# Performance work log

Hardware: AMD Instinct MI355X
Metric: run time of the kernel (lower is better)

## Reference

```python
import jax, jax.numpy as jnp
import numpy as np

B, S, H, NH = 2, 1024, 1024, 16
SE, E = 512, 1024
NEXP, TOPK, FF = 8, 2, 2048
HD = H // NH
EPS = 1e-6
THETA = 10000.0
NEG = -1e9


def _rms(x, w):
    return x * jax.lax.rsqrt(jnp.mean(x * x, axis=-1, keepdims=True) + EPS) * w


def _rope(q, k, pos):
    # q,k: [B,S,NH,HD]; pos: [B,S] int
    inv = 1.0 / (THETA ** (jnp.arange(0, HD, 2, dtype=jnp.float32) / HD))
    f = pos[..., None].astype(jnp.float32) * inv            # [B,S,HD/2]
    emb = jnp.concatenate([f, f], axis=-1)                  # [B,S,HD]
    cos = jnp.cos(emb)[:, :, None, :]
    sin = jnp.sin(emb)[:, :, None, :]
    def rot(x):
        x1, x2 = jnp.split(x, 2, axis=-1)
        return jnp.concatenate([-x2, x1], axis=-1)
    return q * cos + rot(q) * sin, k * cos + rot(k) * sin


def _forward(hidden_states, encoder_hidden_states,
             in_ln_w, wq, wk, wv, wo,
             c_norm_w, cq_w, cq_b, ck_w, ck_b, cv_w, cv_b, co_w, co_b,
             post_ln_w, gate_w, w1, w2, w3,
             position_ids, encoder_attention_mask):
    x = hidden_states

    # ---- self-attention (RMSNorm pre-norm, RoPE, causal) ----
    res = x
    h = _rms(x, in_ln_w)
    q = (h @ wq.T).reshape(B, S, NH, HD)
    k = (h @ wk.T).reshape(B, S, NH, HD)
    v = (h @ wv.T).reshape(B, S, NH, HD)
    q, k = _rope(q, k, position_ids)
    scores = jnp.einsum('bqhd,bkhd->bhqk', q, k) / np.sqrt(HD)
    causal = jnp.tril(jnp.ones((S, S), dtype=bool))
    scores = jnp.where(causal, scores, NEG)
    attn = jax.nn.softmax(scores, axis=-1)
    o = jnp.einsum('bhqk,bkhd->bqhd', attn, v).reshape(B, S, H) @ wo.T
    x = res + o

    # ---- cross-attention block (RMSNorm, MHA with kdim=vdim=E, bias) ----
    res = x
    h = _rms(x, c_norm_w)
    cq = (h @ cq_w.T + cq_b).reshape(B, S, NH, HD)
    ck = (encoder_hidden_states @ ck_w.T + ck_b).reshape(B, SE, NH, HD)
    cv = (encoder_hidden_states @ cv_w.T + cv_b).reshape(B, SE, NH, HD)
    sc = jnp.einsum('bqhd,bkhd->bhqk', cq, ck) / np.sqrt(HD)
    pad = (encoder_attention_mask == 0)                     # key_padding_mask
    sc = jnp.where(pad[:, None, None, :], NEG, sc)
    ca = jax.nn.softmax(sc, axis=-1)
    o = jnp.einsum('bhqk,bkhd->bqhd', ca, cv).reshape(B, S, H) @ co_w.T + co_b
    x = res + o

    # ---- block-sparse MoE FFN (top-2 routing, SwiGLU experts) ----
    res = x
    h = _rms(x, post_ln_w).reshape(-1, H)                   # [T,H], T=B*S
    logits = h @ gate_w.T                                    # [T,NEXP]
    probs = jax.nn.softmax(logits, axis=-1)
    topv, topi = jax.lax.top_k(probs, TOPK)                  # [T,TOPK]
    topv = topv / jnp.sum(topv, axis=-1, keepdims=True)
    out = jnp.zeros_like(h)
    for e in range(NEXP):  # fixed small expert loop
        we = jnp.sum(jnp.where(topi == e, topv, 0.0), axis=-1)   # [T]
        ff = (jax.nn.silu(h @ w1[e].T) * (h @ w3[e].T)) @ w2[e].T
        out = out + we[:, None] * ff
    x = res + out.reshape(B, S, H)
    return x


def setup_inputs() -> dict:
    key = jax.random.key(0)
    ks = jax.random.split(key, 24)
    sc = 0.02
    d = {
        'hidden_states': jax.random.normal(ks[0], (B, S, H), jnp.float32),
        'position_ids': jnp.broadcast_to(jnp.arange(S, dtype=jnp.int64), (B, S)),
        'encoder_hidden_states': jax.random.normal(ks[1], (B, SE, E), jnp.float32),
        'encoder_attention_mask': jnp.ones((B, SE), jnp.int64),
        'in_ln_w': jnp.ones((H,), jnp.float32),
        'wq': jax.random.normal(ks[2], (H, H), jnp.float32) * sc,
        'wk': jax.random.normal(ks[3], (H, H), jnp.float32) * sc,
        'wv': jax.random.normal(ks[4], (H, H), jnp.float32) * sc,
        'wo': jax.random.normal(ks[5], (H, H), jnp.float32) * sc,
        'c_norm_w': jnp.ones((H,), jnp.float32),
        'cq_w': jax.random.normal(ks[6], (H, H), jnp.float32) * sc,
        'cq_b': jnp.zeros((H,), jnp.float32),
        'ck_w': jax.random.normal(ks[7], (H, E), jnp.float32) * sc,
        'ck_b': jnp.zeros((H,), jnp.float32),
        'cv_w': jax.random.normal(ks[8], (H, E), jnp.float32) * sc,
        'cv_b': jnp.zeros((H,), jnp.float32),
        'co_w': jax.random.normal(ks[9], (H, H), jnp.float32) * sc,
        'co_b': jnp.zeros((H,), jnp.float32),
        'post_ln_w': jnp.ones((H,), jnp.float32),
        'gate_w': jax.random.normal(ks[10], (NEXP, H), jnp.float32) * sc,
        'w1': jax.random.normal(ks[11], (NEXP, FF, H), jnp.float32) * sc,
        'w2': jax.random.normal(ks[12], (NEXP, H, FF), jnp.float32) * sc,
        'w3': jax.random.normal(ks[13], (NEXP, FF, H), jnp.float32) * sc,
    }
    return d


def reference(hidden_states, position_ids, encoder_hidden_states, encoder_attention_mask,
              in_ln_w, wq, wk, wv, wo,
              c_norm_w, cq_w, cq_b, ck_w, ck_b, cv_w, cv_b, co_w, co_b,
              post_ln_w, gate_w, w1, w2, w3):
    return _forward(hidden_states, encoder_hidden_states,
                    in_ln_w, wq, wk, wv, wo,
                    c_norm_w, cq_w, cq_b, ck_w, ck_b, cv_w, cv_b, co_w, co_b,
                    post_ln_w, gate_w, w1, w2, w3,
                    position_ids, encoder_attention_mask)
```

## Files before the change

### kernel.cpp

```cpp
#include <hip/hip_runtime.h>

#define B_    2
#define S_    1024
#define H_    1024
#define NH_   16
#define HD_   64
#define SE_   512
#define E_    1024
#define NEXP_ 8
#define FF_   2048
#define T_    (B_*S_)
#define TE_   (B_*SE_)
#define PERM_MAX 6400
#define MAXRT 48

typedef short v8s __attribute__((ext_vector_type(8)));
typedef short v4s __attribute__((ext_vector_type(4)));
typedef float v4f __attribute__((ext_vector_type(4)));
typedef _Float16 v8h __attribute__((ext_vector_type(8)));
typedef _Float16 v4h __attribute__((ext_vector_type(4)));

__device__ __forceinline__ unsigned short f2b(float f) {
  unsigned int u = __float_as_uint(f);
  u = (u + 0x7FFFu + ((u >> 16) & 1u)) >> 16;
  return (unsigned short)u;
}
__device__ __forceinline__ float b2f(unsigned short h) {
  return __uint_as_float(((unsigned int)h) << 16);
}

__device__ __forceinline__ void g2l16(const void* g, void* l) {
  __builtin_amdgcn_global_load_lds(
      (const __attribute__((address_space(1))) unsigned int*)g,
      (__attribute__((address_space(3))) unsigned int*)l, 16, 0, 0);
}

__global__ void detect_kern(const int* __restrict__ pos, const int* __restrict__ msk,
                            int* __restrict__ flags) {
  if (threadIdx.x == 0) {
    flags[0] = (pos[1] == 1) ? 0 : 1;
    flags[1] = (msk[1] == 1) ? 0 : 1;
  }
}

__global__ __launch_bounds__(256)
void split_kern(const float* __restrict__ x, _Float16* __restrict__ oh,
                _Float16* __restrict__ ol, int n8) {
  int i = blockIdx.x * 256 + threadIdx.x;
  if (i >= n8) return;
  v4f a = *(const v4f*)&x[i * 8];
  v4f b = *(const v4f*)&x[i * 8 + 4];
  v8h hv, lv;
  #pragma unroll
  for (int j = 0; j < 8; ++j) {
    float v = j < 4 ? a[j] : b[j - 4];
    _Float16 hh = (_Float16)v;
    hv[j] = hh; lv[j] = (_Float16)(v - (float)hh);
  }
  *(v8h*)&oh[i * 8] = hv;
  *(v8h*)&ol[i * 8] = lv;
}

__global__ __launch_bounds__(256)
void rmsnorm_hl_kern(const float* __restrict__ x, const float* __restrict__ w,
                     _Float16* __restrict__ yh, _Float16* __restrict__ yl) {
  int row = blockIdx.x, tid = threadIdx.x;
  const float* xr = x + (long)row * 1024;
  v4f v = *(const v4f*)&xr[tid * 4];
  float ss = v[0]*v[0] + v[1]*v[1] + v[2]*v[2] + v[3]*v[3];
  #pragma unroll
  for (int off = 32; off; off >>= 1) ss += __shfl_xor(ss, off);
  __shared__ float sw[4];
  if ((tid & 63) == 0) sw[tid >> 6] = ss;
  __syncthreads();
  float tot = sw[0] + sw[1] + sw[2] + sw[3];
  float rs = rsqrtf(tot * (1.0f / 1024.0f) + 1e-6f);
  const float* wr = w + tid * 4;
  v4h oh, ol;
  #pragma unroll
  for (int j = 0; j < 4; ++j) {
    float f = v[j] * rs * wr[j];
    _Float16 hh = (_Float16)f;
    oh[j] = hh; ol[j] = (_Float16)(f - (float)hh);
  }
  *(v4h*)&yh[(long)row * 1024 + tid * 4] = oh;
  *(v4h*)&yl[(long)row * 1024 + tid * 4] = ol;
}

__global__ __launch_bounds__(256)
void rmsnorm_kern(const float* __restrict__ x, const float* __restrict__ w,
                  unsigned short* __restrict__ y) {
  int row = blockIdx.x, tid = threadIdx.x;
  const float* xr = x + (long)row * 1024;
  v4f v = *(const v4f*)&xr[tid * 4];
  float ss = v[0]*v[0] + v[1]*v[1] + v[2]*v[2] + v[3]*v[3];
  #pragma unroll
  for (int off = 32; off; off >>= 1) ss += __shfl_xor(ss, off);
  __shared__ float sw[4];
  if ((tid & 63) == 0) sw[tid >> 6] = ss;
  __syncthreads();
  float tot = sw[0] + sw[1] + sw[2] + sw[3];
  float rs = rsqrtf(tot * (1.0f / 1024.0f) + 1e-6f);
  const float* wr = w + tid * 4;
  v4s o;
  #pragma unroll
  for (int j = 0; j < 4; ++j) o[j] = (short)f2b(v[j] * rs * wr[j]);
  *(v4s*)&y[(long)row * 1024 + tid * 4] = o;
}

__global__ __launch_bounds__(256)
void cvt_kern(const float* __restrict__ x, unsigned short* __restrict__ y, int n4) {
  int i = blockIdx.x * 256 + threadIdx.x;
  if (i >= n4) return;
  v4f v = *(const v4f*)&x[i * 4];
  v4s o;
  #pragma unroll
  for (int j = 0; j < 4; ++j) o[j] = (short)f2b(v[j]);
  *(v4s*)&y[i * 4] = o;
}

__global__ __launch_bounds__(256)
void rope_split_kern(float* __restrict__ q, const float* __restrict__ k,
                     _Float16* __restrict__ kh, _Float16* __restrict__ kl,
                     const int* __restrict__ pos, const int* __restrict__ flags) {
  int g = blockIdx.x * 256 + threadIdx.x;
  int d = g & 31;
  int h = (g >> 5) & 15;
  int s = (g >> 9) & (S_ - 1);
  int b = g >> 19;
  long base = (((long)(b * S_ + s)) * NH_ + h) * HD_;
  int pidx = b * S_ + s;
  int pv = pos[flags[0] ? (pidx << 1) : pidx];
  float p = (float)pv;
  float inv = powf(10000.0f, -(float)d * (1.0f / 32.0f));
  float f = p * inv;
  float sn = sinf(f), cs = cosf(f);
  float q1 = q[base + d], q2 = q[base + d + 32];
  q[base + d]      = q1 * cs - q2 * sn;
  q[base + d + 32] = q2 * cs + q1 * sn;
  float k1 = k[base + d], k2 = k[base + d + 32];
  float kr1 = k1 * cs - k2 * sn;
  float kr2 = k2 * cs + k1 * sn;
  _Float16 hh = (_Float16)kr1;
  kh[base + d] = hh; kl[base + d] = (_Float16)(kr1 - (float)hh);
  hh = (_Float16)kr2;
  kh[base + d + 32] = hh; kl[base + d + 32] = (_Float16)(kr2 - (float)hh);
}

__global__ __launch_bounds__(256)
void vtrans_kern(const float* __restrict__ vf, _Float16* __restrict__ vth,
                 _Float16* __restrict__ vtl, int Sk) {
  int kb = blockIdx.x, bh = blockIdx.y;
  int b = bh >> 4, h = bh & 15;
  int t = threadIdx.x;
  __shared__ float tile[64][65];
  int key = t >> 2, dsub = (t & 3) * 16;
  const float* src = vf + (((long)(b * Sk + kb * 64 + key)) * NH_ + h) * HD_ + dsub;
  #pragma unroll
  for (int j = 0; j < 16; j += 4) *(v4f*)&tile[key][dsub + j] = *(const v4f*)&src[j];
  __syncthreads();
  int d = t >> 2, ksub = (t & 3) * 16;
  v8h hv0, lv0, hv1, lv1;
  #pragma unroll
  for (int j = 0; j < 16; ++j) {
    float v = tile[ksub + j][d];
    _Float16 hh = (_Float16)v;
    if (j < 8) { hv0[j] = hh; lv0[j] = (_Float16)(v - (float)hh); }
    else       { hv1[j - 8] = hh; lv1[j - 8] = (_Float16)(v - (float)hh); }
  }
  long ob = (((long)(b * NH_ + h)) * HD_ + d) * Sk + kb * 64 + ksub;
  *(v8h*)&vth[ob] = hv0; *(v8h*)&vth[ob + 8] = hv1;
  *(v8h*)&vtl[ob] = lv0; *(v8h*)&vtl[ob + 8] = lv1;
}

struct ZArg {
  const _Float16 *Ah, *Al, *Bh, *Bl;
  const float *bias, *resid;
  float *Cf;
  _Float16 *Ch, *Cl;
  int M;
};

__global__ __launch_bounds__(256)
void gemm_hl(ZArg z0, ZArg z1, ZArg z2, int K) {
  ZArg za = blockIdx.z == 0 ? z0 : (blockIdx.z == 1 ? z1 : z2);
  int row0 = blockIdx.x * 128;
  if (row0 >= za.M) return;
  int col0 = blockIdx.y * 64;
  int tid = threadIdx.x, lane = tid & 63, w = tid >> 6;
  int lr = lane & 15, lg = lane >> 4;
  int wr = w >> 1, wc = w & 1;

  __shared__ _Float16 Ah_s[128 * 32], Al_s[128 * 32];
  __shared__ _Float16 Bh_s[64 * 32], Bl_s[64 * 32];

  int av0 = w * 64 + lane, av1 = (w + 4) * 64 + lane;
  int ar0 = av0 >> 2, as0 = av0 & 3;
  int ar1 = av1 >> 2, as1 = av1 & 3;
  int bv = w * 64 + lane;
  int br = bv >> 2, bs = bv & 3;
  const _Float16* ga0h = za.Ah + (long)(row0 + ar0) * K + as0 * 8;
  const _Float16* ga0l = za.Al + (long)(row0 + ar0) * K + as0 * 8;
  const _Float16* ga1h = za.Ah + (long)(row0 + ar1) * K + as1 * 8;
  const _Float16* ga1l = za.Al + (long)(row0 + ar1) * K + as1 * 8;
  const _Float16* gbh  = za.Bh + (long)(col0 + br) * K + bs * 8;
  const _Float16* gbl  = za.Bl + (long)(col0 + br) * K + bs * 8;

  v4f acc[4][2] = {};

  for (int k0 = 0; k0 < K; k0 += 32) {
    __syncthreads();
    g2l16(ga0h + k0, (char*)Ah_s + w * 1024);
    g2l16(ga1h + k0, (char*)Ah_s + (w + 4) * 1024);
    g2l16(ga0l + k0, (char*)Al_s + w * 1024);
    g2l16(ga1l + k0, (char*)Al_s + (w + 4) * 1024);
    g2l16(gbh + k0, (char*)Bh_s + w * 1024);
    g2l16(gbl + k0, (char*)Bl_s + w * 1024);
    __syncthreads();

    v8h ah[4], al[4], bh[2], bl[2];
    #pragma unroll
    for (int m = 0; m < 4; ++m) {
      int off = (wr * 64 + m * 16 + lr) * 64 + lg * 16;
      ah[m] = *(const v8h*)((char*)Ah_s + off);
      al[m] = *(const v8h*)((char*)Al_s + off);
    }
    #pragma unroll
    for (int n = 0; n < 2; ++n) {
      int off = (wc * 32 + n * 16 + lr) * 64 + lg * 16;
      bh[n] = *(const v8h*)((char*)Bh_s + off);
      bl[n] = *(const v8h*)((char*)Bl_s + off);
    }
    #pragma unroll
    for (int m = 0; m < 4; ++m)
      #pragma unroll
      for (int n = 0; n < 2; ++n) {
        acc[m][n] = __builtin_amdgcn_mfma_f32_16x16x32_f16(ah[m], bh[n], acc[m][n], 0, 0, 0);
        acc[m][n] = __builtin_amdgcn_mfma_f32_16x16x32_f16(ah[m], bl[n], acc[m][n], 0, 0, 0);
        acc[m][n] = __builtin_amdgcn_mfma_f32_16x16x32_f16(al[m], bh[n], acc[m][n], 0, 0, 0);
      }
  }

  #pragma unroll
  for (int m = 0; m < 4; ++m) {
    int rbase = row0 + wr * 64 + m * 16 + lg * 4;
    #pragma unroll
    for (int n = 0; n < 2; ++n) {
      int gcol = col0 + wc * 32 + n * 16 + lr;
      float bb = za.bias ? za.bias[gcol] : 0.0f;
      #pragma unroll
      for (int rr = 0; rr < 4; ++rr) {
        long idx = (long)(rbase + rr) * 1024 + gcol;
        float v = acc[m][n][rr] + bb;
        if (za.Cf) {
          za.Cf[idx] = za.resid ? (za.resid[idx] + v) : v;
        } else {
          _Float16 hh = (_Float16)v;
          za.Ch[idx] = hh;
          za.Cl[idx] = (_Float16)(v - (float)hh);
        }
      }
    }
  }
}

template<bool CAUSAL>
__global__ __launch_bounds__(256)
void attn_hl(const float* __restrict__ Q,
             const _Float16* __restrict__ Khg, const _Float16* __restrict__ Klg,
             const _Float16* __restrict__ Vhg, const _Float16* __restrict__ Vlg,
             _Float16* __restrict__ Oh, _Float16* __restrict__ Ol,
             const int* __restrict__ mask, const int* __restrict__ flags,
             int Sq, int Sk, float qscale) {
  int qt = blockIdx.x, bh = blockIdx.y;
  int b = bh >> 4, h = bh & 15;
  int tid = threadIdx.x, lane = tid & 63, w = tid >> 6;
  int lr = lane & 15, lg = lane >> 4;
  int q0 = qt * 64;
  int mf = (!CAUSAL && mask) ? flags[1] : 0;
  int swz = lr & 7;

  __shared__ _Float16 Kh_s[64 * 64], Kl_s[64 * 64];
  __shared__ _Float16 Vh_s[64 * 64], Vl_s[64 * 64];
  __shared__ _Float16 Psh[4][16][72], Psl[4][16][72];

  v8h qh[2], ql[2];
  {
    long qbase = ((long)(b * Sq + q0 + w * 16 + lr) * NH_ + h) * HD_;
    #pragma unroll
    for (int kk = 0; kk < 2; ++kk) {
      v4f f0 = *(const v4f*)&Q[qbase + kk * 32 + lg * 8];
      v4f f1 = *(const v4f*)&Q[qbase + kk * 32 + lg * 8 + 4];
      #pragma unroll
      for (int j = 0; j < 8; ++j) {
        float f = (j < 4 ? f0[j] : f1[j - 4]) * qscale;
        _Float16 hh = (_Float16)f;
        qh[kk][j] = hh;
        ql[kk][j] = (_Float16)(f - (float)hh);
      }
    }
  }
  v4f of[4] = {};
  float m4[4], l4[4];
  #pragma unroll
  for (int i = 0; i < 4; ++i) { m4[i] = -3e38f; l4[i] = 0.0f; }

  int nkt = CAUSAL ? (qt + 1) : (Sk >> 6);
  for (int kt = 0; kt < nkt; ++kt) {
    __syncthreads();
    #pragma unroll
    for (int i = 0; i < 2; ++i) {
      int c = w + i * 4;
      int v = c * 64 + lane;
      int row = v >> 3, c8 = v & 7;
      int sc = (c8 ^ (row & 7)) << 3;
      long kb = ((long)(b * Sk + kt * 64 + row) * NH_ + h) * HD_ + sc;
      g2l16(Khg + kb, (char*)Kh_s + c * 1024);
      g2l16(Klg + kb, (char*)Kl_s + c * 1024);
      long vb = ((long)(b * NH_ + h) * HD_ + row) * Sk + kt * 64 + sc;
      g2l16(Vhg + vb, (char*)Vh_s + c * 1024);
      g2l16(Vlg + vb, (char*)Vl_s + c * 1024);
    }
    __syncthreads();

    v4f sf[4] = {};
    #pragma unroll
    for (int kk = 0; kk < 2; ++kk)
      #pragma unroll
      for (int n = 0; n < 4; ++n) {
        int off = (n * 16 + lr) * 128 + ((((kk << 2) | lg) ^ swz) << 4);
        v8h kbh = *(const v8h*)((char*)Kh_s + off);
        v8h kbl = *(const v8h*)((char*)Kl_s + off);
        sf[n] = __builtin_amdgcn_mfma_f32_16x16x32_f16(qh[kk], kbh, sf[n], 0, 0, 0);
        sf[n] = __builtin_amdgcn_mfma_f32_16x16x32_f16(qh[kk], kbl, sf[n], 0, 0, 0);
        sf[n] = __builtin_amdgcn_mfma_f32_16x16x32_f16(ql[kk], kbh, sf[n], 0, 0, 0);
      }

    if constexpr (CAUSAL) {
      if (kt == qt) {
        #pragma unroll
        for (int n = 0; n < 4; ++n) {
          int kcol = kt * 64 + n * 16 + lr;
          #pragma unroll
          for (int rr = 0; rr < 4; ++rr) {
            int qr = q0 + w * 16 + lg * 4 + rr;
            if (kcol > qr) sf[n][rr] = -1e9f;
          }
        }
      }
    } else {
      if (mask) {
        #pragma unroll
        for (int n = 0; n < 4; ++n) {
          int kcol = kt * 64 + n * 16 + lr;
          int mi = b * Sk + kcol;
          if (mask[mf ? (mi << 1) : mi] == 0) {
            #pragma unroll
            for (int rr = 0; rr < 4; ++rr) sf[n][rr] = -1e9f;
          }
        }
      }
    }

    float al[4];
    #pragma unroll
    for (int rr = 0; rr < 4; ++rr) {
      float mx = fmaxf(fmaxf(sf[0][rr], sf[1][rr]), fmaxf(sf[2][rr], sf[3][rr]));
      #pragma unroll
      for (int off = 8; off; off >>= 1) mx = fmaxf(mx, __shfl_xor(mx, off));
      float mn = fmaxf(m4[rr], mx);
      al[rr] = __expf(m4[rr] - mn);
      m4[rr] = mn;
      float rs = 0.0f;
      #pragma unroll
      for (int n = 0; n < 4; ++n) {
        float pv = __expf(sf[n][rr] - mn);
        sf[n][rr] = pv;
        rs += pv;
      }
      #pragma unroll
      for (int off = 8; off; off >>= 1) rs += __shfl_xor(rs, off);
      l4[rr] = l4[rr] * al[rr] + rs;
    }

    #pragma unroll
    for (int n = 0; n < 4; ++n)
      #pragma unroll
      for (int rr = 0; rr < 4; ++rr) {
        of[n][rr] *= al[rr];
        float pv = sf[n][rr];
        _Float16 ph = (_Float16)pv;
        Psh[w][lg * 4 + rr][n * 16 + lr] = ph;
        Psl[w][lg * 4 + rr][n * 16 + lr] = (_Float16)(pv - (float)ph);
      }
    __syncthreads();

    #pragma unroll
    for (int kc = 0; kc < 2; ++kc) {
      v8h pah = *(const v8h*)&Psh[w][lr][kc * 32 + lg * 8];
      v8h pal = *(const v8h*)&Psl[w][lr][kc * 32 + lg * 8];
      #pragma unroll
      for (int n = 0; n < 4; ++n) {
        int off = (n * 16 + lr) * 128 + ((((kc << 2) | lg) ^ swz) << 4);
        v8h vbh = *(const v8h*)((char*)Vh_s + off);
        v8h vbl = *(const v8h*)((char*)Vl_s + off);
        of[n] = __builtin_amdgcn_mfma_f32_16x16x32_f16(pah, vbh, of[n], 0, 0, 0);
        of[n] = __builtin_amdgcn_mfma_f32_16x16x32_f16(pah, vbl, of[n], 0, 0, 0);
        of[n] = __builtin_amdgcn_mfma_f32_16x16x32_f16(pal, vbh, of[n], 0, 0, 0);
      }
    }
  }

  #pragma unroll
  for (int rr = 0; rr < 4; ++rr) {
    int qr = q0 + w * 16 + lg * 4 + rr;
    float inv = 1.0f / l4[rr];
    long ob = (long)(b * Sq + qr) * 1024 + h * 64;
    #pragma unroll
    for (int n = 0; n < 4; ++n) {
      float v = of[n][rr] * inv;
      _Float16 hh = (_Float16)v;
      Oh[ob + n * 16 + lr] = hh;
      Ol[ob + n * 16 + lr] = (_Float16)(v - (float)hh);
    }
  }
}

__global__ __launch_bounds__(256)
void moe_gemm1(const unsigned short* __restrict__ A,
               const unsigned short* __restrict__ B1,
               const unsigned short* __restrict__ B2,
               unsigned short* __restrict__ Cb,
               const int* __restrict__ tm_e, const int* __restrict__ tm_slot,
               const int* __restrict__ ntl, const int* __restrict__ perm) {
  int tile = blockIdx.x;
  if (tile >= ntl[0]) return;
  int e = tm_e[tile];
  int row0 = tm_slot[tile];
  const unsigned short* Bp1 = B1 + (long)e * (FF_ * H_);
  const unsigned short* Bp2 = B2 + (long)e * (FF_ * H_);
  int col0 = blockIdx.y * 64;
  int tid = threadIdx.x, lane = tid & 63, w = tid >> 6;
  int lr = lane & 15, lg = lane >> 4;
  int wr = w >> 1, wc = w & 1;

  __shared__ unsigned short As[128 * 32];
  __shared__ unsigned short Bs1[64 * 32];
  __shared__ unsigned short Bs2[64 * 32];

  const unsigned short* ga[2];
  #pragma unroll
  for (int i = 0; i < 2; ++i) {
    int c = i * 256 + tid;
    int r = c >> 2, sub = c & 3;
    int tok = perm[row0 + r];
    ga[i] = A + (long)(tok < 0 ? 0 : tok) * H_ + sub * 8;
  }
  int rb = tid >> 2, subb = (tid & 3) * 8;
  const unsigned short* gb1 = Bp1 + (long)(col0 + rb) * H_ + subb;
  const unsigned short* gb2 = Bp2 + (long)(col0 + rb) * H_ + subb;

  v4f acc[4][2] = {};
  v4f acc2[4][2] = {};

  for (int k0 = 0; k0 < H_; k0 += 32) {
    __syncthreads();
    #pragma unroll
    for (int i = 0; i < 2; ++i)
      g2l16(ga[i] + k0, As + (size_t)(i * 256 + w * 64) * 8);
    g2l16(gb1 + k0, Bs1 + (size_t)(w * 64) * 8);
    g2l16(gb2 + k0, Bs2 + (size_t)(w * 64) * 8);
    __syncthreads();

    v8s a[4], b[2];
    #pragma unroll
    for (int m = 0; m < 4; ++m) a[m] = *(const v8s*)&As[(wr * 64 + m * 16 + lr) * 32 + lg * 8];
    #pragma unroll
    for (int n = 0; n < 2; ++n) b[n] = *(const v8s*)&Bs1[(wc * 32 + n * 16 + lr) * 32 + lg * 8];
    #pragma unroll
    for (int m = 0; m < 4; ++m)
      #pragma unroll
      for (int n = 0; n < 2; ++n)
        acc[m][n] = __builtin_amdgcn_mfma_f32_16x16x32_bf16(a[m], b[n], acc[m][n], 0, 0, 0);
    #pragma unroll
    for (int n = 0; n < 2; ++n) b[n] = *(const v8s*)&Bs2[(wc * 32 + n * 16 + lr) * 32 + lg * 8];
    #pragma unroll
    for (int m = 0; m < 4; ++m)
      #pragma unroll
      for (int n = 0; n < 2; ++n)
        acc2[m][n] = __builtin_amdgcn_mfma_f32_16x16x32_bf16(a[m], b[n], acc2[m][n], 0, 0, 0);
  }

  #pragma unroll
  for (int m = 0; m < 4; ++m) {
    int grow = row0 + wr * 64 + m * 16 + lg * 4;
    #pragma unroll
    for (int n = 0; n < 2; ++n) {
      int gcol = col0 + wc * 32 + n * 16 + lr;
      #pragma unroll
      for (int rr = 0; rr < 4; ++rr) {
        float v = acc[m][n][rr];
        float g = v / (1.0f + __expf(-v));
        Cb[(long)(grow + rr) * FF_ + gcol] = f2b(g * acc2[m][n][rr]);
      }
    }
  }
}

__global__ __launch_bounds__(256)
void moe_gemm2(const unsigned short* __restrict__ A,
               const unsigned short* __restrict__ B,
               float* __restrict__ Cf,
               const int* __restrict__ tm_e, const int* __restrict__ tm_slot,
               const int* __restrict__ ntl,
               const int* __restrict__ perm, const float* __restrict__ pwgt) {
  int tile = blockIdx.x;
  if (tile >= ntl[0]) return;
  int e = tm_e[tile];
  int row0 = tm_slot[tile];
  const unsigned short* Bp = B + (long)e * (H_ * FF_);
  int col0 = blockIdx.y * 128;
  int tid = threadIdx.x, lane = tid & 63, w = tid >> 6;
  int lr = lane & 15, lg = lane >> 4;
  int wr = w >> 1, wc = w & 1;

  __shared__ unsigned short As[128 * 32];
  __shared__ unsigned short Bs[128 * 32];

  const unsigned short* ga[2];
  const unsigned short* gb[2];
  #pragma unroll
  for (int i = 0; i < 2; ++i) {
    int c = i * 256 + tid;
    int r = c >> 2, sub = c & 3;
    ga[i] = A + (long)(row0 + r) * FF_ + sub * 8;
    gb[i] = Bp + (long)(col0 + r) * FF_ + sub * 8;
  }

  v4f acc[4][4] = {};

  for (int k0 = 0; k0 < FF_; k0 += 32) {
    __syncthreads();
    #pragma unroll
    for (int i = 0; i < 2; ++i) {
      g2l16(ga[i] + k0, As + (size_t)(i * 256 + w * 64) * 8);
      g2l16(gb[i] + k0, Bs + (size_t)(i * 256 + w * 64) * 8);
    }
    __syncthreads();

    v8s a[4], b[4];
    #pragma unroll
    for (int m = 0; m < 4; ++m) a[m] = *(const v8s*)&As[(wr * 64 + m * 16 + lr) * 32 + lg * 8];
    #pragma unroll
    for (int n = 0; n < 4; ++n) b[n] = *(const v8s*)&Bs[(wc * 64 + n * 16 + lr) * 32 + lg * 8];
    #pragma unroll
    for (int m = 0; m < 4; ++m)
      #pragma unroll
      for (int n = 0; n < 4; ++n)
        acc[m][n] = __builtin_amdgcn_mfma_f32_16x16x32_bf16(a[m], b[n], acc[m][n], 0, 0, 0);
  }

  #pragma unroll
  for (int m = 0; m < 4; ++m) {
    int grow = row0 + wr * 64 + m * 16 + lg * 4;
    #pragma unroll
    for (int rr = 0; rr < 4; ++rr) {
      int tok = perm[grow + rr];
      if (tok < 0) continue;
      float pw = pwgt[grow + rr];
      #pragma unroll
      for (int n = 0; n < 4; ++n) {
        int gcol = col0 + wc * 64 + n * 16 + lr;
        atomicAdd(&Cf[(long)tok * H_ + gcol], acc[m][n][rr] * pw);
      }
    }
  }
}

__global__ __launch_bounds__(64)
void router_kern(const float* __restrict__ x, const float* __restrict__ w,
                 const float* __restrict__ gw,
                 int* __restrict__ topi, float* __restrict__ topw,
                 int* __restrict__ counts) {
  int t = blockIdx.x, lane = threadIdx.x;
  const float* xr = x + (long)t * 1024;
  float vals[16];
  float ss = 0.0f;
  #pragma unroll
  for (int i = 0; i < 16; ++i) { float v = xr[lane + i * 64]; vals[i] = v; ss += v * v; }
  #pragma unroll
  for (int off = 32; off; off >>= 1) ss += __shfl_xor(ss, off);
  float rs = rsqrtf(ss * (1.0f / 1024.0f) + 1e-6f);
  #pragma unroll
  for (int i = 0; i < 16; ++i) vals[i] *= rs * w[lane + i * 64];
  float lgts[8];
  #pragma unroll
  for (int e = 0; e < 8; ++e) {
    const float* g = gw + e * 1024;
    float s = 0.0f;
    #pragma unroll
    for (int i = 0; i < 16; ++i) s += vals[i] * g[lane + i * 64];
    #pragma unroll
    for (int off = 32; off; off >>= 1) s += __shfl_xor(s, off);
    lgts[e] = s;
  }
  int i1 = 0; float l1 = lgts[0];
  #pragma unroll
  for (int e = 1; e < 8; ++e) if (lgts[e] > l1) { l1 = lgts[e]; i1 = e; }
  int i2 = -1; float l2 = -3e38f;
  #pragma unroll
  for (int e = 0; e < 8; ++e) if (e != i1 && lgts[e] > l2) { l2 = lgts[e]; i2 = e; }
  float w1 = 1.0f / (1.0f + __expf(l2 - l1));
  if (lane == 0) {
    topi[t * 2] = i1; topi[t * 2 + 1] = i2;
    topw[t * 2] = w1; topw[t * 2 + 1] = 1.0f - w1;
    atomicAdd(&counts[i1], 1);
    atomicAdd(&counts[i2], 1);
  }
}

__global__ __launch_bounds__(256)
void finalize_kern(const int* __restrict__ counts, int* __restrict__ poff,
                   int* __restrict__ tm_e, int* __restrict__ tm_slot,
                   int* __restrict__ ntl, int* __restrict__ perm) {
  __shared__ int stot;
  if (threadIdx.x == 0) {
    int off = 0, nt = 0;
    for (int e = 0; e < 8; ++e) {
      poff[e] = off;
      int c = counts[e];
      int ntE = (c + 127) >> 7;
      for (int i = 0; i < ntE; ++i) { tm_e[nt] = e; tm_slot[nt] = off + i * 128; ++nt; }
      off += ntE * 128;
    }
    ntl[0] = nt; ntl[1] = off;
    stot = off;
  }
  __syncthreads();
  for (int s = threadIdx.x; s < stot; s += 256) perm[s] = -1;
}

__global__ __launch_bounds__(256)
void scatter_kern(const int* __restrict__ topi, const float* __restrict__ topw,
                  const int* __restrict__ poff, int* __restrict__ cursor,
                  int* __restrict__ perm, float* __restrict__ pwgt) {
  int t = blockIdx.x * 256 + threadIdx.x;
  if (t >= T_) return;
  #pragma unroll
  for (int kk = 0; kk < 2; ++kk) {
    int e = topi[t * 2 + kk];
    int pos = atomicAdd(&cursor[e], 1);
    int slot = poff[e] + pos;
    perm[slot] = t;
    pwgt[slot] = topw[t * 2 + kk];
  }
}

extern "C" void kernel_launch(void* const* d_in, const int* in_sizes, int n_in,
                              void* d_out, int out_size, void* d_ws, size_t ws_size,
                              hipStream_t stream) {
  (void)in_sizes; (void)n_in; (void)out_size; (void)ws_size;
  const float* x_in  = (const float*)d_in[0];
  const int*  posids = (const int*)d_in[1];
  const float* enc   = (const float*)d_in[2];
  const int*  emask  = (const int*)d_in[3];
  const float* inln  = (const float*)d_in[4];
  const float* wq    = (const float*)d_in[5];
  const float* wk    = (const float*)d_in[6];
  const float* wv    = (const float*)d_in[7];
  const float* wo    = (const float*)d_in[8];
  const float* cnorm = (const float*)d_in[9];
  const float* cqw   = (const float*)d_in[10];
  const float* cqb   = (const float*)d_in[11];
  const float* ckw   = (const float*)d_in[12];
  const float* ckb   = (const float*)d_in[13];
  const float* cvw   = (const float*)d_in[14];
  const float* cvb   = (const float*)d_in[15];
  const float* cow   = (const float*)d_in[16];
  const float* cob   = (const float*)d_in[17];
  const float* pln   = (const float*)d_in[18];
  const float* gatew = (const float*)d_in[19];
  const float* w1    = (const float*)d_in[20];
  const float* w2    = (const float*)d_in[21];
  const float* w3    = (const float*)d_in[22];
  float* out = (float*)d_out;

  char* p = (char*)d_ws;
  auto alloc = [&](size_t bytes) -> char* {
    char* r = p;
    p += (bytes + 255) & ~(size_t)255;
    return r;
  };
  const size_t MB = 1024 * 1024;
  char* A1 = alloc(4 * MB);
  char* A2 = alloc(4 * MB);
  char* Bq = alloc(8 * MB);
  char* Bk = alloc(8 * MB);
  char* Bv = alloc(8 * MB);
  char* C1 = alloc(4 * MB);
  char* C2 = alloc(4 * MB);
  char* D1 = alloc(4 * MB);
  char* D2 = alloc(4 * MB);
  float* x1 = (float*)alloc(8 * MB);
  float* x2 = (float*)alloc(8 * MB);
  unsigned short* h3b = (unsigned short*)alloc(4 * MB);
  _Float16* ench = (_Float16*)alloc(2 * MB);
  _Float16* encl = (_Float16*)alloc(2 * MB);
  int*   meta    = (int*)alloc(4 * (8 + 8 + 8 + 2 + 2 + MAXRT + MAXRT));
  int*   counts  = meta;
  int*   cursor  = meta + 8;
  int*   poff    = meta + 16;
  int*   ntl     = meta + 24;
  int*   flags   = meta + 26;
  int*   tm_e    = meta + 28;
  int*   tm_slot = meta + 28 + MAXRT;
  int*   topi    = (int*)alloc((size_t)T_ * 2 * 4);
  float* topw    = (float*)alloc((size_t)T_ * 2 * 4);
  int*   perm    = (int*)alloc((size_t)PERM_MAX * 4);
  float* pwgt    = (float*)alloc((size_t)PERM_MAX * 4);
  unsigned short* w1b = (unsigned short*)alloc((size_t)NEXP_ * FF_ * H_ * 2);
  unsigned short* w3b = (unsigned short*)alloc((size_t)NEXP_ * FF_ * H_ * 2);
  unsigned short* w2b = (unsigned short*)alloc((size_t)NEXP_ * H_ * FF_ * 2);

  _Float16 *hh = (_Float16*)A1, *hl = (_Float16*)A2;
  _Float16 *oh = (_Float16*)A1, *ol = (_Float16*)A2;
  _Float16 *ckh = (_Float16*)A1, *ckl = (_Float16*)A2;
  float* qf = (float*)Bq;  float* cqf = (float*)Bq;
  float* kf = (float*)Bk;
  _Float16 *cvth = (_Float16*)Bk, *cvtl = (_Float16*)(Bk + 4 * MB);
  float* vf = (float*)Bv;  float* cvf = (float*)Bv;
  _Float16 *kh = (_Float16*)C1, *kl = (_Float16*)C2;
  _Float16 *h2h = (_Float16*)C1, *h2l = (_Float16*)C2;
  _Float16 *vth = (_Float16*)D1, *vtl = (_Float16*)D2;
  _Float16 *coh = (_Float16*)D1, *col = (_Float16*)D2;
  unsigned short* ffh = (unsigned short*)Bq;
  _Float16* wsp = (_Float16*)w1b;
  auto wsph = [&](int i) { return wsp + (size_t)i * 2097152; };
  auto wspl = [&](int i) { return wsp + (size_t)i * 2097152 + 1048576; };

  dim3 blk(256);
  const int WN8 = H_ * H_ / 8;

  detect_kern<<<1, 64, 0, stream>>>(posids, emask, flags);

  const float* wlist[8] = {wq, wk, wv, wo, cqw, ckw, cvw, cow};
  for (int i = 0; i < 8; ++i)
    split_kern<<<(WN8 + 255) / 256, blk, 0, stream>>>(wlist[i], wsph(i), wspl(i), WN8);
  split_kern<<<(TE_ * E_ / 8 + 255) / 256, blk, 0, stream>>>(enc, ench, encl, TE_ * E_ / 8);

  rmsnorm_hl_kern<<<T_, blk, 0, stream>>>(x_in, inln, hh, hl);
  {
    ZArg zq = {hh, hl, wsph(0), wspl(0), nullptr, nullptr, qf, nullptr, nullptr, 2048};
    ZArg zk = {hh, hl, wsph(1), wspl(1), nullptr, nullptr, kf, nullptr, nullptr, 2048};
    ZArg zv = {hh, hl, wsph(2), wspl(2), nullptr, nullptr, vf, nullptr, nullptr, 2048};
    gemm_hl<<<dim3(16, 16, 3), blk, 0, stream>>>(zq, zk, zv, 1024);
  }
  rope_split_kern<<<(B_ * S_ * NH_ * 32) / 256, blk, 0, stream>>>(qf, kf, kh, kl, posids, flags);
  vtrans_kern<<<dim3(16, 32), blk, 0, stream>>>(vf, vth, vtl, 1024);
  attn_hl<true><<<dim3(16, 32), blk, 0, stream>>>(
      qf, kh, kl, vth, vtl, oh, ol, nullptr, flags, 1024, 1024, 0.125f);
  {
    ZArg zo = {oh, ol, wsph(3), wspl(3), nullptr, x_in, x1, nullptr, nullptr, 2048};
    gemm_hl<<<dim3(16, 16, 1), blk, 0, stream>>>(zo, zo, zo, 1024);
  }

  rmsnorm_hl_kern<<<T_, blk, 0, stream>>>(x1, cnorm, h2h, h2l);
  {
    ZArg zcq = {h2h, h2l, wsph(4), wspl(4), cqb, nullptr, cqf, nullptr, nullptr, 2048};
    ZArg zck = {ench, encl, wsph(5), wspl(5), ckb, nullptr, nullptr, ckh, ckl, 1024};
    ZArg zcv = {ench, encl, wsph(6), wspl(6), cvb, nullptr, cvf, nullptr, nullptr, 1024};
    gemm_hl<<<dim3(16, 16, 3), blk, 0, stream>>>(zcq, zck, zcv, 1024);
  }
  vtrans_kern<<<dim3(8, 32), blk, 0, stream>>>(cvf, cvth, cvtl, 512);
  attn_hl<false><<<dim3(16, 32), blk, 0, stream>>>(
      cqf, ckh, ckl, cvth, cvtl, coh, col, emask, flags, 1024, 512, 0.125f);
  {
    ZArg zco = {coh, col, wsph(7), wspl(7), cob, x1, x2, nullptr, nullptr, 2048};
    gemm_hl<<<dim3(16, 16, 1), blk, 0, stream>>>(zco, zco, zco, 1024);
  }

  cvt_kern<<<(NEXP_ * FF_ * H_ / 4 + 255) / 256, blk, 0, stream>>>(w1, w1b, NEXP_ * FF_ * H_ / 4);
  cvt_kern<<<(NEXP_ * FF_ * H_ / 4 + 255) / 256, blk, 0, stream>>>(w3, w3b, NEXP_ * FF_ * H_ / 4);
  cvt_kern<<<(NEXP_ * H_ * FF_ / 4 + 255) / 256, blk, 0, stream>>>(w2, w2b, NEXP_ * H_ * FF_ / 4);
  rmsnorm_kern<<<T_, blk, 0, stream>>>(x2, pln, h3b);
  hipMemsetAsync(meta, 0, 64, stream);
  router_kern<<<T_, dim3(64), 0, stream>>>(x2, pln, gatew, topi, topw, counts);
  finalize_kern<<<1, blk, 0, stream>>>(counts, poff, tm_e, tm_slot, ntl, perm);
  scatter_kern<<<(T_ + 255) / 256, blk, 0, stream>>>(topi, topw, poff, cursor, perm, pwgt);
  moe_gemm1<<<dim3(MAXRT, FF_ / 64), blk, 0, stream>>>(
      h3b, w1b, w3b, ffh, tm_e, tm_slot, ntl, perm);
  hipMemcpyAsync(out, x2, (size_t)T_ * H_ * 4, hipMemcpyDeviceToDevice, stream);
  moe_gemm2<<<dim3(MAXRT, H_ / 128), blk, 0, stream>>>(
      ffh, w2b, out, tm_e, tm_slot, ntl, perm, pwgt);
}
```

Measured before the change: 590.8 us.

## Swizzle LDS layouts and double MoE tile rows to 256 with 512-thread blocks

Applies an XOR swizzle to the 16-byte chunk index in the shared-memory layouts of gemm_hl and both MoE GEMMs, so the MFMA operand reads hit fewer LDS bank conflicts. The MoE GEMMs move to 512-thread blocks covering 256-row expert tiles, with finalize and the grid bound changed to match. Each weight tile is then reused across twice as many tokens, cutting repeated weight traffic. The cost is more padding per expert tile (up to 255 rows) and half as many blocks in the MoE launches, which can leave fewer blocks to fill the GPU.

```diff
diff --git a/kernel.cpp b/kernel.cpp
--- a/kernel.cpp
+++ b/kernel.cpp
@@ -12,7 +12,7 @@
 #define T_    (B_*S_)
 #define TE_   (B_*SE_)
 #define PERM_MAX 6400
-#define MAXRT 48
+#define MAXRT 24
 
 typedef short v8s __attribute__((ext_vector_type(8)));
 typedef short v4s __attribute__((ext_vector_type(4)));
@@ -190,15 +190,16 @@
   int tid = threadIdx.x, lane = tid & 63, w = tid >> 6;
   int lr = lane & 15, lg = lane >> 4;
   int wr = w >> 1, wc = w & 1;
+  int rsw = (lr >> 1) & 3;
 
   __shared__ _Float16 Ah_s[128 * 32], Al_s[128 * 32];
   __shared__ _Float16 Bh_s[64 * 32], Bl_s[64 * 32];
 
   int av0 = w * 64 + lane, av1 = (w + 4) * 64 + lane;
-  int ar0 = av0 >> 2, as0 = av0 & 3;
-  int ar1 = av1 >> 2, as1 = av1 & 3;
+  int ar0 = av0 >> 2, as0 = (av0 & 3) ^ ((ar0 >> 1) & 3);
+  int ar1 = av1 >> 2, as1 = (av1 & 3) ^ ((ar1 >> 1) & 3);
   int bv = w * 64 + lane;
-  int br = bv >> 2, bs = bv & 3;
+  int br = bv >> 2, bs = (bv & 3) ^ ((br >> 1) & 3);
   const _Float16* ga0h = za.Ah + (long)(row0 + ar0) * K + as0 * 8;
   const _Float16* ga0l = za.Al + (long)(row0 + ar0) * K + as0 * 8;
   const _Float16* ga1h = za.Ah + (long)(row0 + ar1) * K + as1 * 8;
@@ -221,13 +222,13 @@
     v8h ah[4], al[4], bh[2], bl[2];
     #pragma unroll
     for (int m = 0; m < 4; ++m) {
-      int off = (wr * 64 + m * 16 + lr) * 64 + lg * 16;
+      int off = (wr * 64 + m * 16 + lr) * 64 + ((lg ^ rsw) << 4);
       ah[m] = *(const v8h*)((char*)Ah_s + off);
       al[m] = *(const v8h*)((char*)Al_s + off);
     }
     #pragma unroll
     for (int n = 0; n < 2; ++n) {
-      int off = (wc * 32 + n * 16 + lr) * 64 + lg * 16;
+      int off = (wc * 32 + n * 16 + lr) * 64 + ((lg ^ rsw) << 4);
       bh[n] = *(const v8h*)((char*)Bh_s + off);
       bl[n] = *(const v8h*)((char*)Bl_s + off);
     }
@@ -426,7 +427,7 @@
   }
 }
 
-__global__ __launch_bounds__(256)
+__global__ __launch_bounds__(512)
 void moe_gemm1(const unsigned short* __restrict__ A,
                const unsigned short* __restrict__ B1,
                const unsigned short* __restrict__ B2,
@@ -443,22 +444,24 @@
   int tid = threadIdx.x, lane = tid & 63, w = tid >> 6;
   int lr = lane & 15, lg = lane >> 4;
   int wr = w >> 1, wc = w & 1;
-
-  __shared__ unsigned short As[128 * 32];
+  int rsw = (lr >> 1) & 3;
+
+  __shared__ unsigned short As[256 * 32];
   __shared__ unsigned short Bs1[64 * 32];
   __shared__ unsigned short Bs2[64 * 32];
 
   const unsigned short* ga[2];
   #pragma unroll
   for (int i = 0; i < 2; ++i) {
-    int c = i * 256 + tid;
-    int r = c >> 2, sub = c & 3;
+    int c = i * 512 + tid;
+    int r = c >> 2, sub = (c & 3) ^ ((r >> 1) & 3);
     int tok = perm[row0 + r];
     ga[i] = A + (long)(tok < 0 ? 0 : tok) * H_ + sub * 8;
   }
-  int rb = tid >> 2, subb = (tid & 3) * 8;
-  const unsigned short* gb1 = Bp1 + (long)(col0 + rb) * H_ + subb;
-  const unsigned short* gb2 = Bp2 + (long)(col0 + rb) * H_ + subb;
+  int bc = tid & 255;
+  int rb = bc >> 2, sb = (bc & 3) ^ ((rb >> 1) & 3);
+  const unsigned short* gB = (tid < 256 ? Bp1 : Bp2) + (long)(col0 + rb) * H_ + sb * 8;
+  unsigned short* lB = (tid < 256 ? Bs1 : Bs2) + (size_t)((w & 3) * 64) * 8;
 
   v4f acc[4][2] = {};
   v4f acc2[4][2] = {};
@@ -467,28 +470,26 @@
     __syncthreads();
     #pragma unroll
     for (int i = 0; i < 2; ++i)
-      g2l16(ga[i] + k0, As + (size_t)(i * 256 + w * 64) * 8);
-    g2l16(gb1 + k0, Bs1 + (size_t)(w * 64) * 8);
-    g2l16(gb2 + k0, Bs2 + (size_t)(w * 64) * 8);
-    __syncthreads();
-
-    v8s a[4], b[2];
-    #pragma unroll
-    for (int m = 0; m < 4; ++m) a[m] = *(const v8s*)&As[(wr * 64 + m * 16 + lr) * 32 + lg * 8];
-    #pragma unroll
-    for (int n = 0; n < 2; ++n) b[n] = *(const v8s*)&Bs1[(wc * 32 + n * 16 + lr) * 32 + lg * 8];
+      g2l16(ga[i] + k0, As + (size_t)(i * 512 + w * 64) * 8);
+    g2l16(gB + k0, lB);
+    __syncthreads();
+
+    v8s a[4], b1[2], b2[2];
     #pragma unroll
     for (int m = 0; m < 4; ++m)
-      #pragma unroll
-      for (int n = 0; n < 2; ++n)
-        acc[m][n] = __builtin_amdgcn_mfma_f32_16x16x32_bf16(a[m], b[n], acc[m][n], 0, 0, 0);
-    #pragma unroll
-    for (int n = 0; n < 2; ++n) b[n] = *(const v8s*)&Bs2[(wc * 32 + n * 16 + lr) * 32 + lg * 8];
+      a[m] = *(const v8s*)&As[(wr * 64 + m * 16 + lr) * 32 + (lg ^ rsw) * 8];
+    #pragma unroll
+    for (int n = 0; n < 2; ++n) {
+      b1[n] = *(const v8s*)&Bs1[(wc * 32 + n * 16 + lr) * 32 + (lg ^ rsw) * 8];
+      b2[n] = *(const v8s*)&Bs2[(wc * 32 + n * 16 + lr) * 32 + (lg ^ rsw) * 8];
+    }
     #pragma unroll
     for (int m = 0; m < 4; ++m)
       #pragma unroll
-      for (int n = 0; n < 2; ++n)
-        acc2[m][n] = __builtin_amdgcn_mfma_f32_16x16x32_bf16(a[m], b[n], acc2[m][n], 0, 0, 0);
+      for (int n = 0; n < 2; ++n) {
+        acc[m][n]  = __builtin_amdgcn_mfma_f32_16x16x32_bf16(a[m], b1[n], acc[m][n], 0, 0, 0);
+        acc2[m][n] = __builtin_amdgcn_mfma_f32_16x16x32_bf16(a[m], b2[n], acc2[m][n], 0, 0, 0);
+      }
   }
 
   #pragma unroll
@@ -507,7 +508,7 @@
   }
 }
 
-__global__ __launch_bounds__(256)
+__global__ __launch_bounds__(512)
 void moe_gemm2(const unsigned short* __restrict__ A,
                const unsigned short* __restrict__ B,
                float* __restrict__ Cf,
@@ -523,36 +524,38 @@
   int tid = threadIdx.x, lane = tid & 63, w = tid >> 6;
   int lr = lane & 15, lg = lane >> 4;
   int wr = w >> 1, wc = w & 1;
-
-  __shared__ unsigned short As[128 * 32];
+  int rsw = (lr >> 1) & 3;
+
+  __shared__ unsigned short As[256 * 32];
   __shared__ unsigned short Bs[128 * 32];
 
   const unsigned short* ga[2];
-  const unsigned short* gb[2];
   #pragma unroll
   for (int i = 0; i < 2; ++i) {
-    int c = i * 256 + tid;
-    int r = c >> 2, sub = c & 3;
+    int c = i * 512 + tid;
+    int r = c >> 2, sub = (c & 3) ^ ((r >> 1) & 3);
     ga[i] = A + (long)(row0 + r) * FF_ + sub * 8;
-    gb[i] = Bp + (long)(col0 + r) * FF_ + sub * 8;
-  }
+  }
+  int rb = tid >> 2, sb = (tid & 3) ^ ((rb >> 1) & 3);
+  const unsigned short* gb = Bp + (long)(col0 + rb) * FF_ + sb * 8;
 
   v4f acc[4][4] = {};
 
   for (int k0 = 0; k0 < FF_; k0 += 32) {
     __syncthreads();
     #pragma unroll
-    for (int i = 0; i < 2; ++i) {
-      g2l16(ga[i] + k0, As + (size_t)(i * 256 + w * 64) * 8);
-      g2l16(gb[i] + k0, Bs + (size_t)(i * 256 + w * 64) * 8);
-    }
+    for (int i = 0; i < 2; ++i)
+      g2l16(ga[i] + k0, As + (size_t)(i * 512 + w * 64) * 8);
+    g2l16(gb + k0, Bs + (size_t)(w * 64) * 8);
     __syncthreads();
 
     v8s a[4], b[4];
     #pragma unroll
-    for (int m = 0; m < 4; ++m) a[m] = *(const v8s*)&As[(wr * 64 + m * 16 + lr) * 32 + lg * 8];
-    #pragma unroll
-    for (int n = 0; n < 4; ++n) b[n] = *(const v8s*)&Bs[(wc * 64 + n * 16 + lr) * 32 + lg * 8];
+    for (int m = 0; m < 4; ++m)
+      a[m] = *(const v8s*)&As[(wr * 64 + m * 16 + lr) * 32 + (lg ^ rsw) * 8];
+    #pragma unroll
+    for (int n = 0; n < 4; ++n)
+      b[n] = *(const v8s*)&Bs[(wc * 64 + n * 16 + lr) * 32 + (lg ^ rsw) * 8];
     #pragma unroll
     for (int m = 0; m < 4; ++m)
       #pragma unroll
@@ -629,9 +632,9 @@
     for (int e = 0; e < 8; ++e) {
       poff[e] = off;
       int c = counts[e];
-      int ntE = (c + 127) >> 7;
-      for (int i = 0; i < ntE; ++i) { tm_e[nt] = e; tm_slot[nt] = off + i * 128; ++nt; }
-      off += ntE * 128;
+      int ntE = (c + 255) >> 8;
+      for (int i = 0; i < ntE; ++i) { tm_e[nt] = e; tm_slot[nt] = off + i * 256; ++nt; }
+      off += ntE * 256;
     }
     ntl[0] = nt; ntl[1] = off;
     stot = off;
@@ -787,9 +790,9 @@
   router_kern<<<T_, dim3(64), 0, stream>>>(x2, pln, gatew, topi, topw, counts);
   finalize_kern<<<1, blk, 0, stream>>>(counts, poff, tm_e, tm_slot, ntl, perm);
   scatter_kern<<<(T_ + 255) / 256, blk, 0, stream>>>(topi, topw, poff, cursor, perm, pwgt);
-  moe_gemm1<<<dim3(MAXRT, FF_ / 64), blk, 0, stream>>>(
+  moe_gemm1<<<dim3(MAXRT, FF_ / 64), dim3(512), 0, stream>>>(
       h3b, w1b, w3b, ffh, tm_e, tm_slot, ntl, perm);
   hipMemcpyAsync(out, x2, (size_t)T_ * H_ * 4, hipMemcpyDeviceToDevice, stream);
-  moe_gemm2<<<dim3(MAXRT, H_ / 128), blk, 0, stream>>>(
+  moe_gemm2<<<dim3(MAXRT, H_ / 128), dim3(512), 0, stream>>>(
       ffh, w2b, out, tm_e, tm_slot, ntl, perm, pwgt);
 }
```

Result: no change. 593.8 us (+0.5%).
